# Kernel optimization log

Measured on AMD Instinct MI355X. Metric: run time of the kernel, lower is better.

Reference implementation:

```python
import jax, jax.numpy as jnp
import numpy as np
from jax import lax

C_IN, BATCH, T = 8, 64, 4096   # in_chan is [C, B, T]; T = cfg.l + cfg.pred
D_MODEL, N_STATE, HID = 128, 64, 128  # LS4 encoder dims; HID = cfg.hid_d


def setup_inputs() -> dict:
    key = jax.random.key(0)
    ks = jax.random.split(key, 12)
    s = lambda *sh: 1.0 / np.sqrt(sh[0])
    return {
        "in_chan": jax.random.normal(ks[0], (C_IN, BATCH, T), jnp.float32),
        "h_0": jnp.zeros((1, BATCH, HID), jnp.float32),
        "c_0": jnp.zeros((1, BATCH, HID), jnp.float32),
        # LS4 encoder params
        "W_in": jax.random.normal(ks[1], (C_IN, D_MODEL), jnp.float32) * s(C_IN),
        "b_in": jnp.zeros((D_MODEL,), jnp.float32),
        "log_a": jax.random.normal(ks[2], (D_MODEL, N_STATE), jnp.float32),
        "B_ssm": jax.random.normal(ks[3], (D_MODEL, N_STATE), jnp.float32) * s(N_STATE),
        "C_ssm": jax.random.normal(ks[4], (D_MODEL, N_STATE), jnp.float32) * s(N_STATE),
        "D_ssm": jax.random.normal(ks[5], (D_MODEL,), jnp.float32),
        "W_mu": jax.random.normal(ks[6], (D_MODEL, HID), jnp.float32) * s(D_MODEL),
        "b_mu": jnp.zeros((HID,), jnp.float32),
        # readout (nn.Linear(hidden_dim, 1), xavier init)
        "W_lin": jax.random.normal(ks[7], (HID, 1), jnp.float32) * s(HID),
        "b_lin": jnp.zeros((1,), jnp.float32),
    }


def _encode(data, W_in, b_in, log_a, B_ssm, C_ssm, D_ssm, W_mu, b_mu):
    # data: [B, T, C]. LS4 recurrent (setup_rnn) mode: serial scan over T.
    mask = data[:, -1, :][:, None, :]          # [B, 1, C] (as in torch encode)
    x = data * mask                            # apply mask over channels
    u = x @ W_in + b_in                        # [B, T, d]
    a = jax.nn.sigmoid(log_a)                  # [d, N], stable decay in (0,1)
    h0 = jnp.zeros((u.shape[0], D_MODEL, N_STATE), u.dtype)

    def step(h, u_t):                          # h: [B,d,N], u_t: [B,d]
        h = a * h + B_ssm * u_t[..., None]
        y_t = jnp.sum(C_ssm * h, axis=-1) + D_ssm * u_t
        return h, y_t

    _, ys = lax.scan(step, h0, jnp.swapaxes(u, 0, 1))  # ys: [T, B, d]
    y = jax.nn.gelu(jnp.swapaxes(ys, 0, 1))            # [B, T, d]
    z_mean = y @ W_mu + b_mu                           # [B, T, HID]
    return z_mean                                       # eval-mode z = z_mean


def reference(in_chan, h_0, c_0, W_in, b_in, log_a, B_ssm, C_ssm, D_ssm,
              W_mu, b_mu, W_lin, b_lin):
    data = jnp.transpose(in_chan, (1, 2, 0))   # [B, T, C]
    z = _encode(data, W_in, b_in, log_a, B_ssm, C_ssm, D_ssm, W_mu, b_mu)
    # z[:, -1, :].unsqueeze(2).permute(2, 0, 1) -> [1, B, HID]
    h_n = lax.stop_gradient(z[:, -1, :])[None]  # encode is @torch.no_grad()
    out = jax.nn.sigmoid(h_n @ W_lin + b_lin)   # [1, B, 1]
    return out
```

## Files before the change

kernel.cpp:

```cpp
#include <hip/hip_runtime.h>
#include <hip/hip_bf16.h>
#include <math.h>

#define C_IN    8
#define BATCH   64
#define T_LEN   4096
#define D_MODEL 128
#define N_STATE 64
#define HID     128
#define W_WIN   256
#define TPL     4
#define DPW     4

__device__ float g_Kr[D_MODEL][W_WIN];
__device__ float g_SK[D_MODEL];
__device__ float g_WV[D_MODEL];
__device__ float g_c0;
__device__ float g_ygelu[BATCH * D_MODEL];

__global__ __launch_bounds__(256)
void ls4_kkernel(const float* __restrict__ log_a,
                 const float* __restrict__ B_ssm,
                 const float* __restrict__ C_ssm,
                 const float* __restrict__ W_mu,
                 const float* __restrict__ b_mu,
                 const float* __restrict__ W_lin,
                 const float* __restrict__ b_lin)
{
    __shared__ float kpart[4][W_WIN];
    const int d    = blockIdx.x;
    const int w    = threadIdx.x >> 6;
    const int lane = threadIdx.x & 63;

    const float la = log_a[d * N_STATE + lane];
    const float a  = 1.0f / (1.0f + expf(-la));
    const float CB = B_ssm[d * N_STATE + lane] * C_ssm[d * N_STATE + lane];

    if (w == 0) {
        const float a2 = a * a, a4 = a2 * a2, a8 = a4 * a4, a16 = a8 * a8;
        const float a32 = a16 * a16, a64s = a32 * a32, a128 = a64s * a64s;
        const float a256 = a128 * a128;
        float skl = CB * (1.0f - a256) / (1.0f - a);
#pragma unroll
        for (int off = 32; off; off >>= 1) skl += __shfl_xor(skl, off);
        if (lane == 0) g_SK[d] = skl;
    }
    if (w == 1) {
        float v = fmaf(W_mu[d * HID + lane],      W_lin[lane],
                       W_mu[d * HID + 64 + lane] * W_lin[64 + lane]);
#pragma unroll
        for (int off = 32; off; off >>= 1) v += __shfl_xor(v, off);
        if (lane == 0) g_WV[d] = v;
    }
    if (w == 2 && d == 0) {
        float v = fmaf(b_mu[lane],      W_lin[lane],
                       b_mu[64 + lane] * W_lin[64 + lane]);
#pragma unroll
        for (int off = 32; off; off >>= 1) v += __shfl_xor(v, off);
        if (lane == 0) g_c0 = v + b_lin[0];
    }

    float acc[TPL];
#pragma unroll
    for (int k = 0; k < TPL; ++k) acc[k] = 0.0f;
#pragma unroll 4
    for (int j = 0; j < 16; ++j) {
        const int   n  = (w << 4) + j;
        const float ab = __shfl(a, n);
        const float cb = __shfl(CB, n);
        const float lg = __log2f(ab);
        float p         = exp2f(lg * (float)lane);
        const float a64 = exp2f(lg * 64.0f);
#pragma unroll
        for (int k = 0; k < TPL; ++k) {
            acc[k] = fmaf(cb, p, acc[k]);
            p *= a64;
        }
    }
#pragma unroll
    for (int k = 0; k < TPL; ++k) kpart[w][lane + 64 * k] = acc[k];
    __syncthreads();

    {
        const int tau = threadIdx.x;
        g_Kr[d][(W_WIN - 1) - tau] =
            (kpart[0][tau] + kpart[1][tau]) + (kpart[2][tau] + kpart[3][tau]);
    }
}

__global__ __launch_bounds__(256, 2)
void ls4_scan_kernel(const float* __restrict__ in_chan,
                     const float* __restrict__ W_in,
                     const float* __restrict__ b_in,
                     const float* __restrict__ D_ssm)
{
    const int b    = blockIdx.x >> 3;
    const int dg   = blockIdx.x & 7;
    const int w    = threadIdx.x >> 6;
    const int lane = threadIdx.x & 63;
    const int d0   = dg * 16 + w * DPW;

    const int tb = (T_LEN - W_WIN) + lane * TPL;
    float4 Xa[C_IN];
    float  mask_c[C_IN];
#pragma unroll
    for (int c = 0; c < C_IN; ++c) {
        Xa[c] = *(const float4*)&in_chan[(c * BATCH + b) * T_LEN + tb];
        mask_c[c] = in_chan[(c * BATCH + b) * T_LEN + (T_LEN - 1)];
    }
    float4 Ka[DPW];
    float  win[DPW][C_IN];
    float  bi[DPW], Dv[DPW], SK[DPW];
#pragma unroll
    for (int kd = 0; kd < DPW; ++kd) {
        const int d = d0 + kd;
        Ka[kd] = *(const float4*)&g_Kr[d][lane * TPL];
#pragma unroll
        for (int c = 0; c < C_IN; ++c) win[kd][c] = W_in[c * D_MODEL + d];
        bi[kd] = b_in[d];
        Dv[kd] = D_ssm[d];
        SK[kd] = g_SK[d];
    }

#pragma unroll
    for (int kd = 0; kd < DPW; ++kd) {
        float wcol[C_IN];
#pragma unroll
        for (int c = 0; c < C_IN; ++c) wcol[c] = mask_c[c] * win[kd][c];

        float u0 = 0.0f, u1 = 0.0f, u2 = 0.0f, u3 = 0.0f;
#pragma unroll
        for (int c = 0; c < C_IN; ++c) {
            u0 = fmaf(Xa[c].x, wcol[c], u0);
            u1 = fmaf(Xa[c].y, wcol[c], u1);
            u2 = fmaf(Xa[c].z, wcol[c], u2);
            u3 = fmaf(Xa[c].w, wcol[c], u3);
        }
        float dot0 = u0 * Ka[kd].x;
        float dot1 = u1 * Ka[kd].y;
        dot0 = fmaf(u2, Ka[kd].z, dot0);
        dot1 = fmaf(u3, Ka[kd].w, dot1);
        float dot = dot0 + dot1;

#pragma unroll
        for (int off = 32; off; off >>= 1) dot += __shfl_xor(dot, off);

        if (lane == 0) {
            float u_last = bi[kd];
#pragma unroll
            for (int c = 0; c < C_IN; ++c) u_last = fmaf(mask_c[c], wcol[c], u_last);
            const float y  = dot + bi[kd] * SK[kd] + Dv[kd] * u_last;
            const float y3 = y * y * y;
            const float g  = 0.5f * y * (1.0f + tanhf(0.79788456080287f * (y + 0.044715f * y3)));
            g_ygelu[b * D_MODEL + (d0 + kd)] = g;
        }
    }
}

__global__ __launch_bounds__(128)
void ls4_head_kernel(float* __restrict__ out)
{
    __shared__ float partial[2];
    const int b   = blockIdx.x;
    const int tid = threadIdx.x;

    float v = g_ygelu[b * D_MODEL + tid] * g_WV[tid];
#pragma unroll
    for (int off = 32; off; off >>= 1) v += __shfl_xor(v, off);
    if ((tid & 63) == 0) partial[tid >> 6] = v;
    __syncthreads();
    if (tid == 0)
        out[b] = 1.0f / (1.0f + expf(-(partial[0] + partial[1] + g_c0)));
}

extern "C" void kernel_launch(void* const* d_in, const int* in_sizes, int n_in,
                              void* d_out, int out_size, void* d_ws, size_t ws_size,
                              hipStream_t stream) {
    const float* in_chan = (const float*)d_in[0];
    const float* W_in  = (const float*)d_in[3];
    const float* b_in  = (const float*)d_in[4];
    const float* log_a = (const float*)d_in[5];
    const float* B_ssm = (const float*)d_in[6];
    const float* C_ssm = (const float*)d_in[7];
    const float* D_ssm = (const float*)d_in[8];
    const float* W_mu  = (const float*)d_in[9];
    const float* b_mu  = (const float*)d_in[10];
    const float* W_lin = (const float*)d_in[11];
    const float* b_lin = (const float*)d_in[12];
    float* out = (float*)d_out;
    (void)d_ws; (void)ws_size; (void)in_sizes; (void)n_in;

    ls4_kkernel<<<D_MODEL, 256, 0, stream>>>(log_a, B_ssm, C_ssm,
                                             W_mu, b_mu, W_lin, b_lin);
    ls4_scan_kernel<<<BATCH * 8, 256, 0, stream>>>(in_chan, W_in, b_in, D_ssm);
    ls4_head_kernel<<<BATCH, 128, 0, stream>>>(out);
}
```

Baseline: 16.88 us.

## Fuse scan and head kernels into one 1024-thread block per batch

Merges the per-channel scan kernel and the readout head kernel into a single kernel where one 1024-thread block handles a whole batch row, keeping GELU outputs in shared memory instead of a global buffer. W_in is staged in shared memory and each wave processes 8 channels. This removes a kernel launch and a global round trip, at the cost of fewer blocks (64) and lower occupancy per CU.

```diff
diff --git a/kernel.cpp b/kernel.cpp
--- a/kernel.cpp
+++ b/kernel.cpp
@@ -10,13 +10,12 @@
 #define HID     128
 #define W_WIN   256
 #define TPL     4
-#define DPW     4
+#define DPW     8
 
 __device__ float g_Kr[D_MODEL][W_WIN];
 __device__ float g_SK[D_MODEL];
 __device__ float g_WV[D_MODEL];
 __device__ float g_c0;
-__device__ float g_ygelu[BATCH * D_MODEL];
 
 __global__ __launch_bounds__(256)
 void ls4_kkernel(const float* __restrict__ log_a,
@@ -88,17 +87,24 @@
     }
 }
 
-__global__ __launch_bounds__(256, 2)
-void ls4_scan_kernel(const float* __restrict__ in_chan,
-                     const float* __restrict__ W_in,
-                     const float* __restrict__ b_in,
-                     const float* __restrict__ D_ssm)
+__global__ __launch_bounds__(1024, 1)
+void ls4_scan_head(const float* __restrict__ in_chan,
+                   const float* __restrict__ W_in,
+                   const float* __restrict__ b_in,
+                   const float* __restrict__ D_ssm,
+                   float* __restrict__ out)
 {
-    const int b    = blockIdx.x >> 3;
-    const int dg   = blockIdx.x & 7;
-    const int w    = threadIdx.x >> 6;
-    const int lane = threadIdx.x & 63;
-    const int d0   = dg * 16 + w * DPW;
+    __shared__ float winsh[C_IN][D_MODEL];
+    __shared__ float ysh[D_MODEL];
+    __shared__ float partial[2];
+
+    const int b    = blockIdx.x;
+    const int tid  = threadIdx.x;
+    const int w    = tid >> 6;
+    const int lane = tid & 63;
+    const int d0   = w * DPW;
+
+    winsh[tid >> 7][tid & (D_MODEL - 1)] = W_in[tid];
 
     const int tb = (T_LEN - W_WIN) + lane * TPL;
     float4 Xa[C_IN];
@@ -108,25 +114,17 @@
         Xa[c] = *(const float4*)&in_chan[(c * BATCH + b) * T_LEN + tb];
         mask_c[c] = in_chan[(c * BATCH + b) * T_LEN + (T_LEN - 1)];
     }
-    float4 Ka[DPW];
-    float  win[DPW][C_IN];
-    float  bi[DPW], Dv[DPW], SK[DPW];
+
+    __syncthreads();
+
 #pragma unroll
     for (int kd = 0; kd < DPW; ++kd) {
         const int d = d0 + kd;
-        Ka[kd] = *(const float4*)&g_Kr[d][lane * TPL];
-#pragma unroll
-        for (int c = 0; c < C_IN; ++c) win[kd][c] = W_in[c * D_MODEL + d];
-        bi[kd] = b_in[d];
-        Dv[kd] = D_ssm[d];
-        SK[kd] = g_SK[d];
-    }
+        const float4 Ka = *(const float4*)&g_Kr[d][lane * TPL];
 
-#pragma unroll
-    for (int kd = 0; kd < DPW; ++kd) {
         float wcol[C_IN];
 #pragma unroll
-        for (int c = 0; c < C_IN; ++c) wcol[c] = mask_c[c] * win[kd][c];
+        for (int c = 0; c < C_IN; ++c) wcol[c] = mask_c[c] * winsh[c][d];
 
         float u0 = 0.0f, u1 = 0.0f, u2 = 0.0f, u3 = 0.0f;
 #pragma unroll
@@ -136,38 +134,34 @@
             u2 = fmaf(Xa[c].z, wcol[c], u2);
             u3 = fmaf(Xa[c].w, wcol[c], u3);
         }
-        float dot0 = u0 * Ka[kd].x;
-        float dot1 = u1 * Ka[kd].y;
-        dot0 = fmaf(u2, Ka[kd].z, dot0);
-        dot1 = fmaf(u3, Ka[kd].w, dot1);
+        float dot0 = u0 * Ka.x;
+        float dot1 = u1 * Ka.y;
+        dot0 = fmaf(u2, Ka.z, dot0);
+        dot1 = fmaf(u3, Ka.w, dot1);
         float dot = dot0 + dot1;
 
 #pragma unroll
         for (int off = 32; off; off >>= 1) dot += __shfl_xor(dot, off);
 
         if (lane == 0) {
-            float u_last = bi[kd];
+            const float biv = b_in[d];
+            float u_last = biv;
 #pragma unroll
             for (int c = 0; c < C_IN; ++c) u_last = fmaf(mask_c[c], wcol[c], u_last);
-            const float y  = dot + bi[kd] * SK[kd] + Dv[kd] * u_last;
+            const float y  = dot + biv * g_SK[d] + D_ssm[d] * u_last;
             const float y3 = y * y * y;
             const float g  = 0.5f * y * (1.0f + tanhf(0.79788456080287f * (y + 0.044715f * y3)));
-            g_ygelu[b * D_MODEL + (d0 + kd)] = g;
+            ysh[d] = g;
         }
     }
-}
+    __syncthreads();
 
-__global__ __launch_bounds__(128)
-void ls4_head_kernel(float* __restrict__ out)
-{
-    __shared__ float partial[2];
-    const int b   = blockIdx.x;
-    const int tid = threadIdx.x;
-
-    float v = g_ygelu[b * D_MODEL + tid] * g_WV[tid];
+    if (tid < D_MODEL) {
+        float v = ysh[tid] * g_WV[tid];
 #pragma unroll
-    for (int off = 32; off; off >>= 1) v += __shfl_xor(v, off);
-    if ((tid & 63) == 0) partial[tid >> 6] = v;
+        for (int off = 32; off; off >>= 1) v += __shfl_xor(v, off);
+        if ((tid & 63) == 0) partial[tid >> 6] = v;
+    }
     __syncthreads();
     if (tid == 0)
         out[b] = 1.0f / (1.0f + expf(-(partial[0] + partial[1] + g_c0)));
@@ -192,6 +186,5 @@
 
     ls4_kkernel<<<D_MODEL, 256, 0, stream>>>(log_a, B_ssm, C_ssm,
                                              W_mu, b_mu, W_lin, b_lin);
-    ls4_scan_kernel<<<BATCH * 8, 256, 0, stream>>>(in_chan, W_in, b_in, D_ssm);
-    ls4_head_kernel<<<BATCH, 128, 0, stream>>>(out);
+    ls4_scan_head<<<BATCH, 1024, 0, stream>>>(in_chan, W_in, b_in, D_ssm, out);
 }
```

Result: slower. 18.68 us (+10.6%).
